# Optimization experiments

Hardware: AMD Instinct MI355X
Metric: run time of the kernel (lower is better)

## Reference

```python
import jax, jax.numpy as jnp
import numpy as np

B, N_ATOMS, N_PROBES, N_EDGES = 4, 1250, 50000, 125000
T, D, SH_DIM, NUM_BASIS = 3, 128, 16, 10
CUTOFF = 4.0
NUM_NEIGHBORS = 20.0


def spherical_harmonics_l3(u):
    """Real spherical harmonics l=0..3, component normalization (||Y_l||^2 = 2l+1 on unit vectors). u: [E,3] unit vectors."""
    x, y, z = u[:, 0], u[:, 1], u[:, 2]
    x2, y2, z2 = x * x, y * y, z * z
    s3 = np.sqrt(3.0)
    s15 = np.sqrt(15.0)
    sh = [
        jnp.ones_like(x),                       # l=0
        s3 * x, s3 * y, s3 * z,                 # l=1
        s15 * x * y,                            # l=2
        s15 * y * z,
        (np.sqrt(5.0) / 2.0) * (3.0 * z2 - 1.0),
        s15 * x * z,
        (s15 / 2.0) * (x2 - y2),
        np.sqrt(35.0 / 8.0) * y * (3.0 * x2 - y2),   # l=3
        np.sqrt(105.0) * x * y * z,
        np.sqrt(21.0 / 8.0) * y * (5.0 * z2 - 1.0),
        (np.sqrt(7.0) / 2.0) * (5.0 * z2 * z - 3.0 * z),
        np.sqrt(21.0 / 8.0) * x * (5.0 * z2 - 1.0),
        (np.sqrt(105.0) / 2.0) * z * (x2 - y2),
        np.sqrt(35.0 / 8.0) * x * (x2 - 3.0 * y2),
    ]
    return jnp.stack(sh, axis=-1)  # [E, 16]


def radial_basis(r):
    """Normalized gaussian radial basis on [0, CUTOFF] (e3nn soft_one_hot_linspace style). r: [E]."""
    centers = jnp.linspace(0.0, CUTOFF, NUM_BASIS)
    step = CUTOFF / (NUM_BASIS - 1)
    diff = (r[:, None] - centers) / step
    return jnp.exp(-diff * diff) * 1.12  # [E, NUM_BASIS]


def setup_inputs() -> dict:
    key = jax.random.key(0)
    ks = jax.random.split(key, 10)
    atom_xyz = 6.0 * jax.random.uniform(ks[0], (B, N_ATOMS, 3), jnp.float32)
    probe_xyz = 6.0 * jax.random.uniform(ks[1], (B, N_PROBES, 3), jnp.float32)
    src = jax.random.randint(ks[2], (B, N_EDGES, 1), 0, N_ATOMS)
    dst = jax.random.randint(ks[3], (B, N_EDGES, 1), 0, N_PROBES)
    probe_edges = jnp.concatenate([src, dst], axis=-1).astype(jnp.int32)
    ped = jax.random.randint(ks[4], (B, N_EDGES, 3), -1, 2).astype(jnp.float32)
    cell = jnp.broadcast_to(6.0 * jnp.eye(3, dtype=jnp.float32), (B, 3, 3)) \
        + 0.05 * jax.random.normal(ks[5], (B, 3, 3), jnp.float32)
    atom_rep = jax.random.normal(ks[6], (T, B * N_ATOMS, D), jnp.float32)
    w1 = 0.3 * jax.random.normal(ks[7], (T, NUM_BASIS, 100), jnp.float32)
    w2 = 0.1 * jax.random.normal(ks[8], (T, 100, SH_DIM), jnp.float32)
    w_out = 0.05 * jax.random.normal(ks[9], (D, 1), jnp.float32)
    return {
        "atom_xyz": atom_xyz, "probe_xyz": probe_xyz, "probe_edges": probe_edges,
        "probe_edges_displacement": ped, "cell": cell,
        "num_nodes": jnp.full((B,), N_ATOMS, jnp.int32),
        "num_probes": jnp.full((B,), N_PROBES, jnp.int32),
        "num_probe_edges": jnp.full((B,), N_EDGES, jnp.int32),
        "atom_rep": atom_rep, "w1": w1, "w2": w2, "w_out": w_out,
    }


def reference(atom_xyz, probe_xyz, probe_edges, probe_edges_displacement, cell,
              num_nodes, num_probes, num_probe_edges, atom_rep, w1, w2, w_out):
    b, n = atom_xyz.shape[:2]
    p = probe_xyz.shape[1]
    atoms = atom_xyz.reshape(-1, 3)          # [b*n, 3]  (unpad_and_cat, equal lengths)
    probes_xyz = probe_xyz.reshape(-1, 3)    # [b*p, 3]
    zero = jnp.zeros((1,), num_nodes.dtype)
    node_off = jnp.cumsum(jnp.concatenate([zero, num_nodes[:-1]]))
    probe_off = jnp.cumsum(jnp.concatenate([zero, num_probes[:-1]]))
    off = jnp.stack([node_off, probe_off], axis=-1)[:, None, :]  # [b,1,2]
    edges = (probe_edges + off).reshape(-1, 2)                   # [E,2]
    src, dst = edges[:, 0], edges[:, 1]
    # fractional shift -> cartesian displacement via per-sample cell (repeat_interleave)
    disp = jnp.einsum('bec,bcd->bed', probe_edges_displacement, cell).reshape(-1, 3)
    vec = probes_xyz[dst] - (atoms[src] + disp)                  # [E,3]
    r = jnp.linalg.norm(vec, axis=1)
    u = vec / jnp.maximum(r, 1e-9)[:, None]
    sh = spherical_harmonics_l3(u)                               # [E,16]
    rb = radial_basis(r)                                         # [E,10]
    P = probes_xyz.shape[0]
    probes = jnp.zeros((P, atom_rep.shape[-1]), atom_xyz.dtype)
    inv_sqrt_nn = 1.0 / np.sqrt(NUM_NEIGHBORS)
    for t in range(atom_rep.shape[0]):  # small fixed number of interaction layers
        h = jax.nn.silu(rb @ w1[t]) @ w2[t]          # radial MLP -> per-edge sh weights [E,16]
        scal = jnp.sum(h * sh, axis=-1)              # contract with edge attr [E]
        msg = atom_rep[t][src] * scal[:, None]       # gather + modulate [E,D]
        probes = probes + jax.ops.segment_sum(msg, dst, num_segments=P) * inv_sqrt_nn
    out = (probes @ w_out)[:, 0].reshape(b, p)       # readout 0e scalar, pad_and_stack
    return out, probes
```

## Files before the change

### kernel.cpp

```cpp
#include <hip/hip_runtime.h>
#include <math.h>

#define B_ 4
#define NA 1250
#define NP 50000
#define NE 125000
#define T_ 3
#define D_ 128
#define SHD 16
#define NB 10
#define HID 100
#define E_TOT (B_*NE)
#define P_TOT (B_*NP)
#define A_TOT (B_*NA)
#define INV_SQRT_NN 0.22360679774997896f
#define SCAN_NBLK ((P_TOT + 1023) / 1024)

#define GRID_N 8192
#define RMAX 24.0f
#define FSTR (T_*SHD)

#define NXCD 8
#define GNW (P_TOT/8)
#define GQ  (GNW/NXCD)
#define ENW ((E_TOT + 255)/256)
#define EQ  (ENW/NXCD)
#define ER  (ENW%NXCD)

typedef float f32x4 __attribute__((ext_vector_type(4)));

__device__ __forceinline__ int exed_swz(int bid) {
    int xcd = bid & 7, idx = bid >> 3;
    return (xcd < ER) ? xcd*(EQ+1) + idx
                      : ER*(EQ+1) + (xcd-ER)*EQ + idx;
}

__global__ __launch_bounds__(256) void build_table_kernel(
    const float* __restrict__ w1, const float* __restrict__ w2,
    float* __restrict__ ftab)
{
    int gid  = blockIdx.x*256 + threadIdx.x;
    int w    = gid >> 6;
    int lane = gid & 63;
    int t  = w >> 13;
    int ri = w & (GRID_N-1);

    float r = (float)ri * (RMAX / (float)(GRID_N-1));
    float rb[NB];
    float rs = r * (9.0f / 4.0f);
    #pragma unroll
    for (int i = 0; i < NB; ++i) {
        float dif = rs - (float)i;
        rb[i] = __expf(-dif*dif) * 1.12f;
    }

    float fk[SHD];
    #pragma unroll
    for (int k = 0; k < SHD; ++k) fk[k] = 0.0f;

    if (lane < 50) {
        #pragma unroll
        for (int jj = 0; jj < 2; ++jj) {
            int j = lane + jj*50;
            float h = 0.0f;
            #pragma unroll
            for (int i = 0; i < NB; ++i)
                h += rb[i] * w1[(size_t)(t*NB + i)*HID + j];
            float s = h / (1.0f + __expf(-h));
            const float* c2 = w2 + (size_t)(t*HID + j)*SHD;
            #pragma unroll
            for (int k = 0; k < SHD; ++k) fk[k] += s * c2[k];
        }
    }

    #pragma unroll
    for (int mask = 1; mask < 64; mask <<= 1) {
        #pragma unroll
        for (int k = 0; k < SHD; ++k) fk[k] += __shfl_xor(fk[k], mask);
    }

    if (lane == 0) {
        float* dstp = ftab + (size_t)ri*FSTR + t*SHD;
        #pragma unroll
        for (int k = 0; k < SHD; ++k) dstp[k] = fk[k];
    }
}

__global__ __launch_bounds__(256) void count_kernel(const int* __restrict__ probe_edges,
                                                    int* __restrict__ counts,
                                                    int* __restrict__ rank)
{
    int e = exed_swz(blockIdx.x)*256 + threadIdx.x;
    if (e >= E_TOT) return;
    int b = e / NE;
    int2 pe = ((const int2*)probe_edges)[e];
    int dst = pe.y + b*NP;
    rank[e] = atomicAdd(&counts[dst], 1);
}

__global__ __launch_bounds__(256) void scan1_kernel(const int* __restrict__ counts,
                                                    int* __restrict__ starts,
                                                    int* __restrict__ bsums)
{
    __shared__ int sd[256];
    int base = blockIdx.x*1024 + threadIdx.x*4;
    int v0 = (base+0 < P_TOT) ? counts[base+0] : 0;
    int v1 = (base+1 < P_TOT) ? counts[base+1] : 0;
    int v2 = (base+2 < P_TOT) ? counts[base+2] : 0;
    int v3 = (base+3 < P_TOT) ? counts[base+3] : 0;
    int s = v0+v1+v2+v3;
    sd[threadIdx.x] = s;
    __syncthreads();
    for (int off = 1; off < 256; off <<= 1) {
        int t = (threadIdx.x >= off) ? sd[threadIdx.x - off] : 0;
        __syncthreads();
        sd[threadIdx.x] += t;
        __syncthreads();
    }
    int excl = sd[threadIdx.x] - s;
    if (base+0 < P_TOT) starts[base+0] = excl;
    if (base+1 < P_TOT) starts[base+1] = excl + v0;
    if (base+2 < P_TOT) starts[base+2] = excl + v0 + v1;
    if (base+3 < P_TOT) starts[base+3] = excl + v0 + v1 + v2;
    if (threadIdx.x == 255) bsums[blockIdx.x] = sd[255];
}

__global__ __launch_bounds__(256) void scan2_kernel(int* __restrict__ bsums, int n)
{
    __shared__ int sd[256];
    int s = (threadIdx.x < n) ? bsums[threadIdx.x] : 0;
    sd[threadIdx.x] = s;
    __syncthreads();
    for (int off = 1; off < 256; off <<= 1) {
        int t = (threadIdx.x >= off) ? sd[threadIdx.x - off] : 0;
        __syncthreads();
        sd[threadIdx.x] += t;
        __syncthreads();
    }
    if (threadIdx.x < n) bsums[threadIdx.x] = sd[threadIdx.x] - s;
}

__global__ __launch_bounds__(256) void scan3_kernel(int* __restrict__ starts,
                                                    const int* __restrict__ bsums)
{
    int add = bsums[blockIdx.x];
    int base = blockIdx.x*1024 + threadIdx.x*4;
    #pragma unroll
    for (int k = 0; k < 4; ++k)
        if (base+k < P_TOT) starts[base+k] += add;
}

__global__ __launch_bounds__(256) void edge_scatter_kernel(
    const float* __restrict__ atom_xyz, const float* __restrict__ probe_xyz,
    const int* __restrict__ probe_edges, const float* __restrict__ ped,
    const float* __restrict__ cell, const float* __restrict__ ftab,
    const int* __restrict__ starts, const int* __restrict__ rank,
    float4* __restrict__ edge4)
{
    int e = exed_swz(blockIdx.x)*256 + threadIdx.x;
    if (e >= E_TOT) return;
    int b  = e / NE;

    int2 pe = ((const int2*)probe_edges)[e];
    int src = pe.x + b * NA;
    int dst = pe.y + b * NP;

    float p0 = __builtin_nontemporal_load(ped + (size_t)e*3 + 0);
    float p1 = __builtin_nontemporal_load(ped + (size_t)e*3 + 1);
    float p2 = __builtin_nontemporal_load(ped + (size_t)e*3 + 2);
    const float* cb = cell + b*9;
    float dx = p0*cb[0] + p1*cb[3] + p2*cb[6];
    float dy = p0*cb[1] + p1*cb[4] + p2*cb[7];
    float dz = p0*cb[2] + p1*cb[5] + p2*cb[8];

    float vx = probe_xyz[(size_t)dst*3+0] - (atom_xyz[(size_t)src*3+0] + dx);
    float vy = probe_xyz[(size_t)dst*3+1] - (atom_xyz[(size_t)src*3+1] + dy);
    float vz = probe_xyz[(size_t)dst*3+2] - (atom_xyz[(size_t)src*3+2] + dz);
    float r = sqrtf(vx*vx + vy*vy + vz*vz);
    float rinv = 1.0f / fmaxf(r, 1e-9f);
    float x = vx*rinv, y = vy*rinv, z = vz*rinv;
    float x2 = x*x, y2 = y*y, z2 = z*z;

    const float S3  = 1.7320508075688772f;
    const float S15 = 3.872983346207417f;
    float sh[SHD];
    sh[0]  = 1.0f;
    sh[1]  = S3 * x;
    sh[2]  = S3 * y;
    sh[3]  = S3 * z;
    sh[4]  = S15 * x * y;
    sh[5]  = S15 * y * z;
    sh[6]  = 1.118033988749895f * (3.0f*z2 - 1.0f);
    sh[7]  = S15 * x * z;
    sh[8]  = 1.9364916731037085f * (x2 - y2);
    sh[9]  = 2.091650066335189f  * y * (3.0f*x2 - y2);
    sh[10] = 10.246950765959598f * x * y * z;
    sh[11] = 1.6201851746019651f * y * (5.0f*z2 - 1.0f);
    sh[12] = 1.3228756555322954f * (5.0f*z2*z - 3.0f*z);
    sh[13] = 1.6201851746019651f * x * (5.0f*z2 - 1.0f);
    sh[14] = 5.123475382979799f  * z * (x2 - y2);
    sh[15] = 2.091650066335189f  * x * (x2 - 3.0f*y2);

    float u = r * ((float)(GRID_N-1) / RMAX);
    int i0 = (int)u;
    i0 = (i0 > GRID_N-2) ? (GRID_N-2) : i0;
    float w = u - (float)i0;
    const float* F0 = ftab + (size_t)i0 * FSTR;
    const float* F1 = F0 + FSTR;

    float sc[T_];
    #pragma unroll
    for (int t = 0; t < T_; ++t) {
        float d0 = 0.0f, d1 = 0.0f;
        #pragma unroll
        for (int k = 0; k < SHD; ++k) {
            d0 += F0[t*SHD + k] * sh[k];
            d1 += F1[t*SHD + k] * sh[k];
        }
        sc[t] = d0 + w * (d1 - d0);
    }

    int pos = starts[dst] + rank[e];
    edge4[pos] = make_float4(sc[0], sc[1], sc[2], __int_as_float(src));
}

__global__ __launch_bounds__(256) void gather_kernel(
    const int* __restrict__ counts, const int* __restrict__ starts,
    const float4* __restrict__ edge4, const float* __restrict__ atom_rep,
    const float* __restrict__ w_out,
    float* __restrict__ out, float* __restrict__ probes)
{
    int lane = threadIdx.x & 63;
    int half = lane >> 5;
    int l    = lane & 31;
    int wv   = threadIdx.x >> 6;
    int blk = (blockIdx.x & 7)*GQ + (blockIdx.x >> 3);
    int p = blk*8 + wv*2 + half;

    int st  = starts[p];
    int cnt = counts[p];

    const float4* rep4 = (const float4*)atom_rep;
    const size_t TS = (size_t)A_TOT * (D_/4);

    float ax = 0.0f, ay = 0.0f, az = 0.0f, aw = 0.0f;

    for (int base = 0; base < cnt; base += 2) {
        int m = cnt - base;
        float4 e0, e1;
        e0 = edge4[st+base];
        if (m > 1) e1 = edge4[st+base+1];

        float4 a00,a01,a02, a10,a11,a12;
        {           size_t ro = (size_t)__float_as_int(e0.w)*(D_/4) + l;
                    a00 = rep4[ro]; a01 = rep4[TS+ro]; a02 = rep4[2*TS+ro]; }
        if (m > 1) { size_t ro = (size_t)__float_as_int(e1.w)*(D_/4) + l;
                    a10 = rep4[ro]; a11 = rep4[TS+ro]; a12 = rep4[2*TS+ro]; }

        ax += e0.x*a00.x + e0.y*a01.x + e0.z*a02.x;
        ay += e0.x*a00.y + e0.y*a01.y + e0.z*a02.y;
        az += e0.x*a00.z + e0.y*a01.z + e0.z*a02.z;
        aw += e0.x*a00.w + e0.y*a01.w + e0.z*a02.w;
        if (m > 1) {
            ax += e1.x*a10.x + e1.y*a11.x + e1.z*a12.x;
            ay += e1.x*a10.y + e1.y*a11.y + e1.z*a12.y;
            az += e1.x*a10.z + e1.y*a11.z + e1.z*a12.z;
            aw += e1.x*a10.w + e1.y*a11.w + e1.z*a12.w;
        }
    }

    ax *= INV_SQRT_NN; ay *= INV_SQRT_NN; az *= INV_SQRT_NN; aw *= INV_SQRT_NN;

    f32x4 v; v.x = ax; v.y = ay; v.z = az; v.w = aw;
    __builtin_nontemporal_store(v, (f32x4*)(probes) + (size_t)p*(D_/4) + l);

    float4 wo = ((const float4*)w_out)[l];
    float ov = ax*wo.x + ay*wo.y + az*wo.z + aw*wo.w;
    #pragma unroll
    for (int off = 16; off > 0; off >>= 1) ov += __shfl_down(ov, off, 32);
    if (l == 0) out[p] = ov;
}

extern "C" void kernel_launch(void* const* d_in, const int* in_sizes, int n_in,
                              void* d_out, int out_size, void* d_ws, size_t ws_size,
                              hipStream_t stream) {
    const float* atom_xyz  = (const float*)d_in[0];
    const float* probe_xyz = (const float*)d_in[1];
    const int*   probe_edges = (const int*)d_in[2];
    const float* ped       = (const float*)d_in[3];
    const float* cell      = (const float*)d_in[4];
    const float* atom_rep  = (const float*)d_in[8];
    const float* w1        = (const float*)d_in[9];
    const float* w2        = (const float*)d_in[10];
    const float* w_out     = (const float*)d_in[11];

    float* out    = (float*)d_out;
    float* probes = out + P_TOT;

    float4* edge4 = (float4*)d_ws;
    float*  ftab  = (float*)(edge4 + E_TOT);
    int* counts   = (int*)(ftab + (size_t)GRID_N*FSTR);
    int* starts   = counts + P_TOT;
    int* bsums    = starts + P_TOT;
    int* rank     = bsums + 256;

    hipMemsetAsync(counts, 0, P_TOT*sizeof(int), stream);

    build_table_kernel<<<(T_*GRID_N)/4, 256, 0, stream>>>(w1, w2, ftab);

    count_kernel<<<ENW, 256, 0, stream>>>(probe_edges, counts, rank);

    scan1_kernel<<<SCAN_NBLK, 256, 0, stream>>>(counts, starts, bsums);
    scan2_kernel<<<1, 256, 0, stream>>>(bsums, SCAN_NBLK);
    scan3_kernel<<<SCAN_NBLK, 256, 0, stream>>>(starts, bsums);

    edge_scatter_kernel<<<ENW, 256, 0, stream>>>(
        atom_xyz, probe_xyz, probe_edges, ped, cell, ftab,
        starts, rank, edge4);

    gather_kernel<<<GNW, 256, 0, stream>>>(
        counts, starts, edge4, atom_rep, w_out, out, probes);
}
```

Before: 275.8 us.

## Fuse table build with counting, drop scan3, persistent gather with prefetch

Merges the radial-table build and the edge-count kernels into one launch, split by block index. Removes the scan3 pass by adding the block offset from bsums wherever a start is read. Converts the gather kernel into a grid-stride persistent loop over 3200 blocks that prefetches the next probe's start, count and first edge record while the current probe is processed. This cuts launch overhead and hides gather latency, at the cost of extra bsums reads and more register pressure in the gather loop.

```diff
diff --git a/kernel.cpp b/kernel.cpp
--- a/kernel.cpp
+++ b/kernel.cpp
@@ -21,11 +21,12 @@
 #define FSTR (T_*SHD)
 
 #define NXCD 8
-#define GNW (P_TOT/8)
-#define GQ  (GNW/NXCD)
 #define ENW ((E_TOT + 255)/256)
 #define EQ  (ENW/NXCD)
 #define ER  (ENW%NXCD)
+#define BT_BLOCKS ((T_*GRID_N)/4)
+#define GB 3200
+#define GSLOTS (GB*8)
 
 typedef float f32x4 __attribute__((ext_vector_type(4)));
 
@@ -35,67 +36,66 @@
                       : ER*(EQ+1) + (xcd-ER)*EQ + idx;
 }
 
-__global__ __launch_bounds__(256) void build_table_kernel(
+__global__ __launch_bounds__(256) void prep_kernel(
     const float* __restrict__ w1, const float* __restrict__ w2,
-    float* __restrict__ ftab)
-{
-    int gid  = blockIdx.x*256 + threadIdx.x;
-    int w    = gid >> 6;
-    int lane = gid & 63;
-    int t  = w >> 13;
-    int ri = w & (GRID_N-1);
-
-    float r = (float)ri * (RMAX / (float)(GRID_N-1));
-    float rb[NB];
-    float rs = r * (9.0f / 4.0f);
-    #pragma unroll
-    for (int i = 0; i < NB; ++i) {
-        float dif = rs - (float)i;
-        rb[i] = __expf(-dif*dif) * 1.12f;
-    }
-
-    float fk[SHD];
-    #pragma unroll
-    for (int k = 0; k < SHD; ++k) fk[k] = 0.0f;
-
-    if (lane < 50) {
-        #pragma unroll
-        for (int jj = 0; jj < 2; ++jj) {
-            int j = lane + jj*50;
-            float h = 0.0f;
+    float* __restrict__ ftab,
+    const int* __restrict__ probe_edges, int* __restrict__ counts,
+    int* __restrict__ rank)
+{
+    if (blockIdx.x < BT_BLOCKS) {
+        int gid  = blockIdx.x*256 + threadIdx.x;
+        int w    = gid >> 6;
+        int lane = gid & 63;
+        int t  = w >> 13;
+        int ri = w & (GRID_N-1);
+
+        float r = (float)ri * (RMAX / (float)(GRID_N-1));
+        float rb[NB];
+        float rs = r * (9.0f / 4.0f);
+        #pragma unroll
+        for (int i = 0; i < NB; ++i) {
+            float dif = rs - (float)i;
+            rb[i] = __expf(-dif*dif) * 1.12f;
+        }
+
+        float fk[SHD];
+        #pragma unroll
+        for (int k = 0; k < SHD; ++k) fk[k] = 0.0f;
+
+        if (lane < 50) {
             #pragma unroll
-            for (int i = 0; i < NB; ++i)
-                h += rb[i] * w1[(size_t)(t*NB + i)*HID + j];
-            float s = h / (1.0f + __expf(-h));
-            const float* c2 = w2 + (size_t)(t*HID + j)*SHD;
+            for (int jj = 0; jj < 2; ++jj) {
+                int j = lane + jj*50;
+                float h = 0.0f;
+                #pragma unroll
+                for (int i = 0; i < NB; ++i)
+                    h += rb[i] * w1[(size_t)(t*NB + i)*HID + j];
+                float s = h / (1.0f + __expf(-h));
+                const float* c2 = w2 + (size_t)(t*HID + j)*SHD;
+                #pragma unroll
+                for (int k = 0; k < SHD; ++k) fk[k] += s * c2[k];
+            }
+        }
+
+        #pragma unroll
+        for (int mask = 1; mask < 64; mask <<= 1) {
             #pragma unroll
-            for (int k = 0; k < SHD; ++k) fk[k] += s * c2[k];
-        }
-    }
-
-    #pragma unroll
-    for (int mask = 1; mask < 64; mask <<= 1) {
-        #pragma unroll
-        for (int k = 0; k < SHD; ++k) fk[k] += __shfl_xor(fk[k], mask);
-    }
-
-    if (lane == 0) {
-        float* dstp = ftab + (size_t)ri*FSTR + t*SHD;
-        #pragma unroll
-        for (int k = 0; k < SHD; ++k) dstp[k] = fk[k];
-    }
-}
-
-__global__ __launch_bounds__(256) void count_kernel(const int* __restrict__ probe_edges,
-                                                    int* __restrict__ counts,
-                                                    int* __restrict__ rank)
-{
-    int e = exed_swz(blockIdx.x)*256 + threadIdx.x;
-    if (e >= E_TOT) return;
-    int b = e / NE;
-    int2 pe = ((const int2*)probe_edges)[e];
-    int dst = pe.y + b*NP;
-    rank[e] = atomicAdd(&counts[dst], 1);
+            for (int k = 0; k < SHD; ++k) fk[k] += __shfl_xor(fk[k], mask);
+        }
+
+        if (lane == 0) {
+            float* dstp = ftab + (size_t)ri*FSTR + t*SHD;
+            #pragma unroll
+            for (int k = 0; k < SHD; ++k) dstp[k] = fk[k];
+        }
+    } else {
+        int e = exed_swz(blockIdx.x - BT_BLOCKS)*256 + threadIdx.x;
+        if (e >= E_TOT) return;
+        int b = e / NE;
+        int2 pe = ((const int2*)probe_edges)[e];
+        int dst = pe.y + b*NP;
+        rank[e] = atomicAdd(&counts[dst], 1);
+    }
 }
 
 __global__ __launch_bounds__(256) void scan1_kernel(const int* __restrict__ counts,
@@ -140,22 +140,12 @@
     if (threadIdx.x < n) bsums[threadIdx.x] = sd[threadIdx.x] - s;
 }
 
-__global__ __launch_bounds__(256) void scan3_kernel(int* __restrict__ starts,
-                                                    const int* __restrict__ bsums)
-{
-    int add = bsums[blockIdx.x];
-    int base = blockIdx.x*1024 + threadIdx.x*4;
-    #pragma unroll
-    for (int k = 0; k < 4; ++k)
-        if (base+k < P_TOT) starts[base+k] += add;
-}
-
 __global__ __launch_bounds__(256) void edge_scatter_kernel(
     const float* __restrict__ atom_xyz, const float* __restrict__ probe_xyz,
     const int* __restrict__ probe_edges, const float* __restrict__ ped,
     const float* __restrict__ cell, const float* __restrict__ ftab,
-    const int* __restrict__ starts, const int* __restrict__ rank,
-    float4* __restrict__ edge4)
+    const int* __restrict__ starts, const int* __restrict__ bsums,
+    const int* __restrict__ rank, float4* __restrict__ edge4)
 {
     int e = exed_swz(blockIdx.x)*256 + threadIdx.x;
     if (e >= E_TOT) return;
@@ -164,6 +154,8 @@
     int2 pe = ((const int2*)probe_edges)[e];
     int src = pe.x + b * NA;
     int dst = pe.y + b * NP;
+
+    int pos = starts[dst] + bsums[dst >> 10] + rank[e];
 
     float p0 = __builtin_nontemporal_load(ped + (size_t)e*3 + 0);
     float p1 = __builtin_nontemporal_load(ped + (size_t)e*3 + 1);
@@ -220,12 +212,12 @@
         sc[t] = d0 + w * (d1 - d0);
     }
 
-    int pos = starts[dst] + rank[e];
     edge4[pos] = make_float4(sc[0], sc[1], sc[2], __int_as_float(src));
 }
 
 __global__ __launch_bounds__(256) void gather_kernel(
     const int* __restrict__ counts, const int* __restrict__ starts,
+    const int* __restrict__ bsums,
     const float4* __restrict__ edge4, const float* __restrict__ atom_rep,
     const float* __restrict__ w_out,
     float* __restrict__ out, float* __restrict__ probes)
@@ -234,51 +226,70 @@
     int half = lane >> 5;
     int l    = lane & 31;
     int wv   = threadIdx.x >> 6;
-    int blk = (blockIdx.x & 7)*GQ + (blockIdx.x >> 3);
-    int p = blk*8 + wv*2 + half;
-
-    int st  = starts[p];
-    int cnt = counts[p];
+    int blk  = (blockIdx.x & 7)*(GB/8) + (blockIdx.x >> 3);
+    int p    = blk*8 + wv*2 + half;
 
     const float4* rep4 = (const float4*)atom_rep;
     const size_t TS = (size_t)A_TOT * (D_/4);
-
-    float ax = 0.0f, ay = 0.0f, az = 0.0f, aw = 0.0f;
-
-    for (int base = 0; base < cnt; base += 2) {
-        int m = cnt - base;
-        float4 e0, e1;
-        e0 = edge4[st+base];
-        if (m > 1) e1 = edge4[st+base+1];
-
-        float4 a00,a01,a02, a10,a11,a12;
-        {           size_t ro = (size_t)__float_as_int(e0.w)*(D_/4) + l;
-                    a00 = rep4[ro]; a01 = rep4[TS+ro]; a02 = rep4[2*TS+ro]; }
-        if (m > 1) { size_t ro = (size_t)__float_as_int(e1.w)*(D_/4) + l;
-                    a10 = rep4[ro]; a11 = rep4[TS+ro]; a12 = rep4[2*TS+ro]; }
-
-        ax += e0.x*a00.x + e0.y*a01.x + e0.z*a02.x;
-        ay += e0.x*a00.y + e0.y*a01.y + e0.z*a02.y;
-        az += e0.x*a00.z + e0.y*a01.z + e0.z*a02.z;
-        aw += e0.x*a00.w + e0.y*a01.w + e0.z*a02.w;
-        if (m > 1) {
-            ax += e1.x*a10.x + e1.y*a11.x + e1.z*a12.x;
-            ay += e1.x*a10.y + e1.y*a11.y + e1.z*a12.y;
-            az += e1.x*a10.z + e1.y*a11.z + e1.z*a12.z;
-            aw += e1.x*a10.w + e1.y*a11.w + e1.z*a12.w;
-        }
-    }
-
-    ax *= INV_SQRT_NN; ay *= INV_SQRT_NN; az *= INV_SQRT_NN; aw *= INV_SQRT_NN;
-
-    f32x4 v; v.x = ax; v.y = ay; v.z = az; v.w = aw;
-    __builtin_nontemporal_store(v, (f32x4*)(probes) + (size_t)p*(D_/4) + l);
-
     float4 wo = ((const float4*)w_out)[l];
-    float ov = ax*wo.x + ay*wo.y + az*wo.z + aw*wo.w;
-    #pragma unroll
-    for (int off = 16; off > 0; off >>= 1) ov += __shfl_down(ov, off, 32);
-    if (l == 0) out[p] = ov;
+
+    int st  = starts[p] + bsums[p >> 10];
+    int cnt = counts[p];
+    float4 e0 = make_float4(0,0,0,0);
+    if (cnt > 0) e0 = edge4[st];
+
+    while (true) {
+        int pn = p + GSLOTS;
+        bool hasNext = (pn < P_TOT);
+        int stn = 0, cntn = 0;
+        if (hasNext) { stn = starts[pn] + bsums[pn >> 10]; cntn = counts[pn]; }
+
+        float ax = 0.0f, ay = 0.0f, az = 0.0f, aw = 0.0f;
+        if (cnt > 0) {
+            size_t ro = (size_t)__float_as_int(e0.w)*(D_/4) + l;
+            float4 a0 = rep4[ro], a1 = rep4[TS+ro], a2 = rep4[2*TS+ro];
+            ax = e0.x*a0.x + e0.y*a1.x + e0.z*a2.x;
+            ay = e0.x*a0.y + e0.y*a1.y + e0.z*a2.y;
+            az = e0.x*a0.z + e0.y*a1.z + e0.z*a2.z;
+            aw = e0.x*a0.w + e0.y*a1.w + e0.z*a2.w;
+            for (int base = 1; base < cnt; base += 2) {
+                int m = cnt - base;
+                float4 f0 = edge4[st+base], f1 = f0;
+                if (m > 1) f1 = edge4[st+base+1];
+                float4 b00,b01,b02, b10,b11,b12;
+                {           size_t r2 = (size_t)__float_as_int(f0.w)*(D_/4) + l;
+                            b00 = rep4[r2]; b01 = rep4[TS+r2]; b02 = rep4[2*TS+r2]; }
+                if (m > 1) { size_t r2 = (size_t)__float_as_int(f1.w)*(D_/4) + l;
+                            b10 = rep4[r2]; b11 = rep4[TS+r2]; b12 = rep4[2*TS+r2]; }
+                ax += f0.x*b00.x + f0.y*b01.x + f0.z*b02.x;
+                ay += f0.x*b00.y + f0.y*b01.y + f0.z*b02.y;
+                az += f0.x*b00.z + f0.y*b01.z + f0.z*b02.z;
+                aw += f0.x*b00.w + f0.y*b01.w + f0.z*b02.w;
+                if (m > 1) {
+                    ax += f1.x*b10.x + f1.y*b11.x + f1.z*b12.x;
+                    ay += f1.x*b10.y + f1.y*b11.y + f1.z*b12.y;
+                    az += f1.x*b10.z + f1.y*b11.z + f1.z*b12.z;
+                    aw += f1.x*b10.w + f1.y*b11.w + f1.z*b12.w;
+                }
+            }
+        }
+
+        float4 e0n = make_float4(0,0,0,0);
+        if (hasNext && cntn > 0) e0n = edge4[stn];
+
+        ax *= INV_SQRT_NN; ay *= INV_SQRT_NN; az *= INV_SQRT_NN; aw *= INV_SQRT_NN;
+
+        f32x4 v; v.x = ax; v.y = ay; v.z = az; v.w = aw;
+        __builtin_nontemporal_store(v, (f32x4*)(probes) + (size_t)p*(D_/4) + l);
+
+        float ov = ax*wo.x + ay*wo.y + az*wo.z + aw*wo.w;
+        #pragma unroll
+        for (int off = 16; off > 0; off >>= 1) ov += __shfl_down(ov, off, 32);
+        if (l == 0) out[p] = ov;
+
+        if (!hasNext) break;
+        p = pn; st = stn; cnt = cntn; e0 = e0n;
+    }
 }
 
 extern "C" void kernel_launch(void* const* d_in, const int* in_sizes, int n_in,
@@ -306,18 +317,16 @@
 
     hipMemsetAsync(counts, 0, P_TOT*sizeof(int), stream);
 
-    build_table_kernel<<<(T_*GRID_N)/4, 256, 0, stream>>>(w1, w2, ftab);
-
-    count_kernel<<<ENW, 256, 0, stream>>>(probe_edges, counts, rank);
+    prep_kernel<<<BT_BLOCKS + ENW, 256, 0, stream>>>(
+        w1, w2, ftab, probe_edges, counts, rank);
 
     scan1_kernel<<<SCAN_NBLK, 256, 0, stream>>>(counts, starts, bsums);
     scan2_kernel<<<1, 256, 0, stream>>>(bsums, SCAN_NBLK);
-    scan3_kernel<<<SCAN_NBLK, 256, 0, stream>>>(starts, bsums);
 
     edge_scatter_kernel<<<ENW, 256, 0, stream>>>(
         atom_xyz, probe_xyz, probe_edges, ped, cell, ftab,
-        starts, rank, edge4);
-
-    gather_kernel<<<GNW, 256, 0, stream>>>(
-        counts, starts, edge4, atom_rep, w_out, out, probes);
-}
+        starts, bsums, rank, edge4);
+
+    gather_kernel<<<GB, 256, 0, stream>>>(
+        counts, starts, bsums, edge4, atom_rep, w_out, out, probes);
+}
```

Measured after the change: 271.2 us. No clear change (-1.7%).
